# Optimization experiments

Measured on AMD Instinct MI355X. Metric: run time of the kernel, lower is better.

The kernel has to match this reference:

```python
import jax, jax.numpy as jnp
import numpy as np

B, D, S, U, H = 2, 1024, 2048, 1024, 16
LN_EPS = 1e-5

def setup_inputs() -> dict:
    key = jax.random.key(0)
    ks = jax.random.split(key, 5)
    std = 0.02
    return {
        "inputs": jax.random.normal(ks[0], (B, D, S), jnp.float32),
        "Wq": jax.random.normal(ks[1], (D, U), jnp.float32) * std,
        "bq": jnp.zeros((U,), jnp.float32),
        "Wk": jax.random.normal(ks[2], (D, U), jnp.float32) * std,
        "bk": jnp.zeros((U,), jnp.float32),
        "Wv": jax.random.normal(ks[3], (D, U), jnp.float32) * std,
        "bv": jnp.zeros((U,), jnp.float32),
        "Wo": jax.random.normal(ks[4], (U, D), jnp.float32) * std,
        "bo": jnp.zeros((D,), jnp.float32),
        "gamma": jnp.ones((D,), jnp.float32),
        "beta": jnp.zeros((D,), jnp.float32),
        "num_heads": H,
    }

def reference(inputs, Wq, bq, Wk, bk, Wv, bv, Wo, bo, gamma, beta, num_heads):
    # inputs: (B, D, S) -> (B, S, D)
    x = jnp.transpose(inputs, (0, 2, 1))
    b, s, d = x.shape

    def proj(W, bias):
        y = jax.nn.relu(x @ W + bias)               # (b, s, U)
        y = y.reshape(b, s, num_heads, -1)
        return jnp.transpose(y, (0, 2, 1, 3))       # (b, h, s, hd)

    Q = proj(Wq, bq)
    K = proj(Wk, bk)
    V = proj(Wv, bv)
    hd = Q.shape[-1]
    scale = 1.0 / np.sqrt(hd).astype(np.float32)

    # Block-wise flash attention in the source is mathematically plain softmax attention
    # (per-block epsilon 1e-10 is negligible); scale applied to Q, no mask, no dropout.
    scores = jnp.einsum('bhid,bhjd->bhij', Q * scale, K)   # (b, h, s, s)
    P = jax.nn.softmax(scores, axis=-1)
    O = jnp.einsum('bhij,bhjd->bhid', P, V)                # (b, h, s, hd)

    O = jnp.transpose(O, (0, 2, 1, 3)).reshape(b, s, -1)   # (b, s, U)
    out = O @ Wo + bo + x                                  # residual add
    mean = jnp.mean(out, axis=-1, keepdims=True)
    var = jnp.var(out, axis=-1, keepdims=True)
    y = (out - mean) * jax.lax.rsqrt(var + LN_EPS) * gamma + beta
    return jnp.transpose(y, (0, 2, 1))                     # (B, D, S)
```

## Files before the change

kernel.cpp:

```cpp
#include <hip/hip_runtime.h>
#include <hip/hip_bf16.h>

typedef __bf16 bf16x8 __attribute__((ext_vector_type(8)));
typedef __bf16 bf16x4 __attribute__((ext_vector_type(4)));
typedef float  f32x4  __attribute__((ext_vector_type(4)));
typedef float  f32x16 __attribute__((ext_vector_type(16)));

#define MFMA16(a, b, c) __builtin_amdgcn_mfma_f32_16x16x32_bf16((a), (b), (c), 0, 0, 0)
#define MFMA32(a, b, c) __builtin_amdgcn_mfma_f32_32x32x16_bf16((a), (b), (c), 0, 0, 0)

namespace {
constexpr int Bb = 2, Dd = 1024, Ss = 2048, Uu = 1024, Hh = 16;
}

#if __has_builtin(__builtin_amdgcn_exp2f)
#define EXP2(x) __builtin_amdgcn_exp2f(x)
#else
#define EXP2(x) __expf((x) * 0.6931471805599453f)
#endif

__device__ __forceinline__ uint32_t pkbf(float a, float b) {
  union { __bf16 h[2]; uint32_t u; } z;
  z.h[0] = (__bf16)a; z.h[1] = (__bf16)b;
  return z.u;
}
#define PLSWAP(a, b) asm("v_permlane32_swap_b32 %0, %1" : "+v"(a), "+v"(b))

__device__ __forceinline__ void gl16(const void* g, void* l) {
  __builtin_amdgcn_global_load_lds((const __attribute__((address_space(1))) uint32_t*)g,
                                   (__attribute__((address_space(3))) uint32_t*)l, 16, 0, 0);
}

#define VMW(n) asm volatile("s_waitcnt vmcnt(" #n ")" ::: "memory")
#define BARRIER_PIN() do { __builtin_amdgcn_s_barrier(); \
  asm volatile("" ::: "memory"); __builtin_amdgcn_sched_barrier(0); } while (0)
#define LGKM0() asm volatile("s_waitcnt lgkmcnt(0)" ::: "memory")

__global__ __launch_bounds__(256) void k_xpose_x(const float* __restrict__ inp,
                                                 __bf16* __restrict__ xb, float* __restrict__ xt) {
  __shared__ __attribute__((aligned(16))) float xs[64][65];
  const int s0 = blockIdx.x * 64, d0 = blockIdx.y * 64, b = blockIdx.z;
  const int t = threadIdx.x;
  {
    const int i = t >> 2, c = (t & 3) * 16;
    const float* src = inp + ((size_t)(b * Dd + d0 + i)) * Ss + s0 + c;
#pragma unroll
    for (int q = 0; q < 4; ++q) {
      const float4 f = *(const float4*)(src + q * 4);
      xs[i][c + q * 4 + 0] = f.x; xs[i][c + q * 4 + 1] = f.y;
      xs[i][c + q * 4 + 2] = f.z; xs[i][c + q * 4 + 3] = f.w;
    }
  }
  __syncthreads();
  {
    const int sl = t >> 2, dc = (t & 3) * 16;
    float* dstf = xt + ((size_t)(b * Ss + s0 + sl)) * Dd + d0 + dc;
    bf16x8 va, vb;
#pragma unroll
    for (int q = 0; q < 4; ++q) {
      float4 f;
      f.x = xs[dc + q * 4 + 0][sl]; f.y = xs[dc + q * 4 + 1][sl];
      f.z = xs[dc + q * 4 + 2][sl]; f.w = xs[dc + q * 4 + 3][sl];
      *(float4*)(dstf + q * 4) = f;
    }
#pragma unroll
    for (int j = 0; j < 8; ++j) { va[j] = (__bf16)xs[dc + j][sl]; vb[j] = (__bf16)xs[dc + 8 + j][sl]; }
    __bf16* dst = xb + ((size_t)(b * Ss + s0 + sl)) * Dd + d0 + dc;
    *(bf16x8*)dst = va;
    *(bf16x8*)(dst + 8) = vb;
  }
}

__global__ __launch_bounds__(256) void k_xpose_w(const float* __restrict__ w0, const float* __restrict__ w1,
                                                 const float* __restrict__ w2, const float* __restrict__ w3,
                                                 __bf16* __restrict__ o0, __bf16* __restrict__ o1,
                                                 __bf16* __restrict__ o2, __bf16* __restrict__ o3) {
  __shared__ __attribute__((aligned(16))) __bf16 ts[64][72];
  const float* src_m; __bf16* dst_m;
  switch (blockIdx.z) {
    case 0: src_m = w0; dst_m = o0; break;
    case 1: src_m = w1; dst_m = o1; break;
    case 2: src_m = w2; dst_m = o2; break;
    default: src_m = w3; dst_m = o3; break;
  }
  const int n0 = blockIdx.x * 64, k0 = blockIdx.y * 64;
  const int t = threadIdx.x;
  {
    const int i = t >> 2, c = (t & 3) * 16;
    const float* src = src_m + (size_t)(k0 + i) * 1024 + n0 + c;
#pragma unroll
    for (int q = 0; q < 4; ++q) {
      const float4 f = *(const float4*)(src + q * 4);
      ts[i][c + q * 4 + 0] = (__bf16)f.x;
      ts[i][c + q * 4 + 1] = (__bf16)f.y;
      ts[i][c + q * 4 + 2] = (__bf16)f.z;
      ts[i][c + q * 4 + 3] = (__bf16)f.w;
    }
  }
  __syncthreads();
  {
    const int nl = t >> 2, kc = (t & 3) * 16;
    bf16x8 va, vb;
#pragma unroll
    for (int j = 0; j < 8; ++j) { va[j] = ts[kc + j][nl]; vb[j] = ts[kc + 8 + j][nl]; }
    __bf16* dst = dst_m + (size_t)(n0 + nl) * 1024 + k0 + kc;
    *(bf16x8*)dst = va;
    *(bf16x8*)(dst + 8) = vb;
  }
}

__global__ __launch_bounds__(512, 2) void k_gemm_qkv8(const __bf16* __restrict__ A,
    const __bf16* __restrict__ W0, const __bf16* __restrict__ W1, const __bf16* __restrict__ W2,
    const float* __restrict__ b0, const float* __restrict__ b1, const float* __restrict__ b2,
    __bf16* __restrict__ Qb, __bf16* __restrict__ Kb, __bf16* __restrict__ Vt) {
  __shared__ __attribute__((aligned(16))) __bf16 As[4][256][32];
  __shared__ __attribute__((aligned(16))) __bf16 Bs[4][256][32];
  const int t = threadIdx.x;
  const int w = t >> 6, l = t & 63, lg = l >> 4, lr = l & 15;
  const int wm = w >> 2, wn = w & 3;
  const int bid = blockIdx.x;
  const int logical = (bid & 7) * 24 + (bid >> 3);
  const int z = logical >> 6;
  const int rem = logical & 63;
  const int n0 = (rem & 3) * 256, m0 = (rem >> 2) * 256;
  const __bf16* Bt = z == 0 ? W0 : z == 1 ? W1 : W2;
  const float* bias = z == 0 ? b0 : z == 1 ? b1 : b2;

  const int srow = t >> 2, sc8 = t & 3, scol = sc8 * 8;
  const int so = ((sc8 + 4 - ((srow >> 1) & 3)) & 3) * 8;
  const __bf16* gaB = A  + ((size_t)(m0 + srow)) * 1024 + so;
  const __bf16* gbB = Bt + ((size_t)(n0 + srow)) * 1024 + so;
#define STG_A(s, h, kt) gl16(gaB + (size_t)(h) * 128 * 1024 + (kt) * 32, &As[s][(h) * 128 + srow][scol])
#define STG_B(s, h, kt) gl16(gbB + (size_t)(h) * 128 * 1024 + (kt) * 32, &Bs[s][(h) * 128 + srow][scol])

  STG_A(0, 0, 0); STG_A(0, 1, 0); STG_B(0, 0, 0); STG_B(0, 1, 0);
  STG_A(1, 0, 1); STG_A(1, 1, 1); STG_B(1, 0, 1); STG_B(1, 1, 1);
  STG_A(2, 0, 2); STG_A(2, 1, 2); STG_B(2, 0, 2); STG_B(2, 1, 2);
  f32x4 acc[8][4] = {};
  VMW(8);
  BARRIER_PIN();

  const int rdc = ((lg + (lr >> 1)) & 3) * 8;
  const __bf16* Abase = &As[0][0][0] + wm * 4096 + lr * 32 + rdc;
  const __bf16* Bbase = &Bs[0][0][0] + wn * 2048 + lr * 32 + rdc;

  for (int kt = 0; kt < 32; ++kt) {
    const int sC = kt & 3, sS = (kt + 3) & 3;
    const __bf16* Ap = Abase + sC * 8192;
    const __bf16* Bp = Bbase + sC * 8192;
    bf16x8 a0, a1, a2, a3, bb0, bb1, bb2, bb3;
    a0 = *(const bf16x8*)(Ap);         a1 = *(const bf16x8*)(Ap + 512);
    a2 = *(const bf16x8*)(Ap + 1024);  a3 = *(const bf16x8*)(Ap + 1536);
    bb0 = *(const bf16x8*)(Bp);        bb1 = *(const bf16x8*)(Bp + 512);
    bb2 = *(const bf16x8*)(Bp + 1024); bb3 = *(const bf16x8*)(Bp + 1536);
    if (kt < 29) { STG_A(sS, 0, kt + 3); STG_A(sS, 1, kt + 3); }
    BARRIER_PIN();
    LGKM0(); __builtin_amdgcn_sched_barrier(0);
    __builtin_amdgcn_s_setprio(1);
    acc[0][0] = MFMA16(a0, bb0, acc[0][0]); acc[0][1] = MFMA16(a0, bb1, acc[0][1]);
    acc[0][2] = MFMA16(a0, bb2, acc[0][2]); acc[0][3] = MFMA16(a0, bb3, acc[0][3]);
    acc[1][0] = MFMA16(a1, bb0, acc[1][0]); acc[1][1] = MFMA16(a1, bb1, acc[1][1]);
    acc[1][2] = MFMA16(a1, bb2, acc[1][2]); acc[1][3] = MFMA16(a1, bb3, acc[1][3]);
    acc[2][0] = MFMA16(a2, bb0, acc[2][0]); acc[2][1] = MFMA16(a2, bb1, acc[2][1]);
    acc[2][2] = MFMA16(a2, bb2, acc[2][2]); acc[2][3] = MFMA16(a2, bb3, acc[2][3]);
    acc[3][0] = MFMA16(a3, bb0, acc[3][0]); acc[3][1] = MFMA16(a3, bb1, acc[3][1]);
    acc[3][2] = MFMA16(a3, bb2, acc[3][2]); acc[3][3] = MFMA16(a3, bb3, acc[3][3]);
    __builtin_amdgcn_s_setprio(0);
    BARRIER_PIN();
    a0 = *(const bf16x8*)(Ap + 2048);  a1 = *(const bf16x8*)(Ap + 2560);
    a2 = *(const bf16x8*)(Ap + 3072);  a3 = *(const bf16x8*)(Ap + 3584);
    if (kt < 29) { STG_B(sS, 0, kt + 3); STG_B(sS, 1, kt + 3); }
    if (kt < 29) { VMW(8); } else if (kt == 29) { VMW(4); } else if (kt == 30) { VMW(0); }
    BARRIER_PIN();
    LGKM0(); __builtin_amdgcn_sched_barrier(0);
    __builtin_amdgcn_s_setprio(1);
    acc[4][0] = MFMA16(a0, bb0, acc[4][0]); acc[4][1] = MFMA16(a0, bb1, acc[4][1]);
    acc[4][2] = MFMA16(a0, bb2, acc[4][2]); acc[4][3] = MFMA16(a0, bb3, acc[4][3]);
    acc[5][0] = MFMA16(a1, bb0, acc[5][0]); acc[5][1] = MFMA16(a1, bb1, acc[5][1]);
    acc[5][2] = MFMA16(a1, bb2, acc[5][2]); acc[5][3] = MFMA16(a1, bb3, acc[5][3]);
    acc[6][0] = MFMA16(a2, bb0, acc[6][0]); acc[6][1] = MFMA16(a2, bb1, acc[6][1]);
    acc[6][2] = MFMA16(a2, bb2, acc[6][2]); acc[6][3] = MFMA16(a2, bb3, acc[6][3]);
    acc[7][0] = MFMA16(a3, bb0, acc[7][0]); acc[7][1] = MFMA16(a3, bb1, acc[7][1]);
    acc[7][2] = MFMA16(a3, bb2, acc[7][2]); acc[7][3] = MFMA16(a3, bb3, acc[7][3]);
    __builtin_amdgcn_s_setprio(0);
    BARRIER_PIN();
  }
#undef STG_A
#undef STG_B

  const int b = m0 >> 11, sb = m0 & 2047;
  __bf16* Ct = &As[0][0][0];
  float bi[4];
#pragma unroll
  for (int j = 0; j < 4; ++j) bi[j] = bias[n0 + wn * 64 + j * 16 + lr];
  if (z < 2) {
    __bf16* out = z == 0 ? Qb : Kb;
    const float scale = z == 0 ? 0.125f * 1.44269504f : 1.0f;
    const int h0 = n0 >> 6;
    for (int c = 0; c < 4; ++c) {
      __syncthreads();
      if (wm == (c >> 1)) {
        const int q = c & 1;
#pragma unroll
        for (int j = 0; j < 4; ++j) {
          const int nl = wn * 64 + j * 16 + lr;
#pragma unroll
          for (int i2 = 0; i2 < 4; ++i2)
#pragma unroll
            for (int r = 0; r < 4; ++r)
              Ct[(i2 * 16 + lg * 4 + r) * 264 + nl] =
                  (__bf16)(fmaxf(acc[q * 4 + i2][j][r] + bi[j], 0.0f) * scale);
        }
      }
      __syncthreads();
#pragma unroll
      for (int u4 = 0; u4 < 4; ++u4) {
        const int u = u4 * 512 + t;
        const int sl = u >> 5, ru = u & 31;
        const int hh = ru >> 3, sg = ru & 7;
        const bf16x8 v = *(const bf16x8*)&Ct[sl * 264 + hh * 64 + sg * 8];
        *(bf16x8*)(out + ((size_t)(b * Hh + h0 + hh) * Ss + sb + c * 64 + sl) * 64 + sg * 8) = v;
      }
    }
  } else {
    for (int c = 0; c < 4; ++c) {
      __syncthreads();
      if (wn == c) {
#pragma unroll
        for (int j = 0; j < 4; ++j) {
          const int nli = j * 16 + lr;
#pragma unroll
          for (int mi = 0; mi < 8; ++mi)
#pragma unroll
            for (int r2 = 0; r2 < 4; r2 += 2) {
              const int ml = wm * 128 + mi * 16 + lg * 4 + r2;
              const uint32_t pk = pkbf(fmaxf(acc[mi][j][r2] + bi[j], 0.0f),
                                       fmaxf(acc[mi][j][r2 + 1] + bi[j], 0.0f));
              *(uint32_t*)&Ct[nli * 264 + ml] = pk;
            }
        }
      }
      __syncthreads();
#pragma unroll
      for (int u4 = 0; u4 < 4; ++u4) {
        const int u = u4 * 512 + t;
        const int nl = u >> 5, sg = u & 31;
        const bf16x8 v = *(const bf16x8*)&Ct[nl * 264 + sg * 8];
        *(bf16x8*)(Vt + (size_t)(b * 1024 + n0 + c * 64 + nl) * Ss + sb + sg * 8) = v;
      }
    }
  }
}

__device__ __forceinline__ int swz_slot(int row, int slot) { return (slot + (row >> 1)) & 3; }

__device__ __forceinline__ void gemm_core(const __bf16* __restrict__ A, const __bf16* __restrict__ Bt,
                                          __bf16 (*__restrict__ As)[128][32], __bf16 (*__restrict__ Bs)[128][32],
                                          int m0, int n0, int t, f32x4 acc[4][4]) {
  const int w = t >> 6, l = t & 63;
  const int wm = (w >> 1) * 64, wn = (w & 1) * 64;
  const int lg = l >> 4, lr = l & 15;
  const int sr = t >> 2, sc8 = t & 3;
  const int so = ((sc8 + 4 - ((sr >> 1) & 3)) & 3) * 8;
  const __bf16* ga = A + (size_t)(m0 + sr) * 1024 + so;
  const __bf16* gb = Bt + (size_t)(n0 + sr) * 1024 + so;
  const int de = sr * 32 + sc8 * 8;
#define STG(bf, kk) { \
    gl16(ga + (kk) * 32,             &As[bf][0][0] + de); \
    gl16(ga + (kk) * 32 + 64 * 1024, &As[bf][0][0] + de + 64 * 32); \
    gl16(gb + (kk) * 32,             &Bs[bf][0][0] + de); \
    gl16(gb + (kk) * 32 + 64 * 1024, &Bs[bf][0][0] + de + 64 * 32); }
  STG(0, 0) STG(1, 1)
  for (int s = 0; s < 32; ++s) {
    if (s < 31) { VMW(4); } else { VMW(0); }
    BARRIER_PIN();
    if (s + 2 < 32) { const int b2 = (s + 2) % 3; STG(b2, s + 2) }
    const int cb = s % 3;
    bf16x8 af[4], bfr[4];
#pragma unroll
    for (int i = 0; i < 4; ++i) { const int rr = wm + i * 16 + lr; af[i]  = *(const bf16x8*)&As[cb][rr][swz_slot(rr, lg) * 8]; }
#pragma unroll
    for (int i = 0; i < 4; ++i) { const int rr = wn + i * 16 + lr; bfr[i] = *(const bf16x8*)&Bs[cb][rr][swz_slot(rr, lg) * 8]; }
#pragma unroll
    for (int i = 0; i < 4; ++i)
#pragma unroll
      for (int j = 0; j < 4; ++j) acc[i][j] = MFMA16(af[i], bfr[j], acc[i][j]);
  }
#undef STG
}

__global__ __launch_bounds__(256) void k_gemm_o(const __bf16* __restrict__ A, const __bf16* __restrict__ Bt,
                                                const float* __restrict__ bias, const float* __restrict__ xt,
                                                float* __restrict__ Wb, float* __restrict__ partials) {
  __shared__ __attribute__((aligned(16))) char smem[49152];
  auto As = (__bf16 (*)[128][32])smem;
  auto Bs = (__bf16 (*)[128][32])(smem + 24576);
  float* Cs = (float*)smem;
  const int flat = blockIdx.x;
  const int logical = (flat & 7) * 32 + (flat >> 3);
  const int n0 = (logical & 7) * 128, m0 = (logical >> 3) * 128;
  const int t = threadIdx.x, w = t >> 6, l = t & 63;
  const int wm = (w >> 1) * 64, wn = (w & 1) * 64;
  const int lg = l >> 4, lr = l & 15;
  f32x4 acc[4][4] = {};
  gemm_core(A, Bt, As, Bs, m0, n0, t, acc);
  const int sub = t & 31, rid0 = t >> 5;
#pragma unroll
  for (int h2 = 0; h2 < 2; ++h2) {
    __syncthreads();
    if ((w >> 1) == h2) {
#pragma unroll
      for (int j = 0; j < 4; ++j) {
        const int nl = wn + j * 16 + lr;
        const float bi = bias[n0 + nl];
#pragma unroll
        for (int i = 0; i < 4; ++i)
#pragma unroll
          for (int r = 0; r < 4; ++r)
            Cs[(i * 16 + lg * 4 + r) * 132 + nl] = acc[i][j][r] + bi;
      }
    }
    __syncthreads();
#pragma unroll
    for (int p = 0; p < 8; ++p) {
      const int row = p * 8 + rid0;
      const int m = m0 + h2 * 64 + row;
      float4 v = *(const float4*)&Cs[row * 132 + sub * 4];
      const float4 x4 = *(const float4*)&xt[(size_t)m * 1024 + n0 + sub * 4];
      v.x += x4.x; v.y += x4.y; v.z += x4.z; v.w += x4.w;
      *(float4*)&Wb[(size_t)m * 1024 + n0 + sub * 4] = v;
      float s = v.x + v.y + v.z + v.w;
      float q = v.x * v.x + v.y * v.y + v.z * v.z + v.w * v.w;
      s += __shfl_xor(s, 1); s += __shfl_xor(s, 2); s += __shfl_xor(s, 4); s += __shfl_xor(s, 8);
      q += __shfl_xor(q, 1); q += __shfl_xor(q, 2); q += __shfl_xor(q, 4); q += __shfl_xor(q, 8);
      if ((sub & 15) == 0) {
        const int ci = (n0 >> 6) + (sub >> 4);
        partials[((size_t)m * 16 + ci) * 2]     = s;
        partials[((size_t)m * 16 + ci) * 2 + 1] = q;
      }
    }
  }
}

__global__ __launch_bounds__(256, 2) void k_attn6(const __bf16* __restrict__ Qg, const __bf16* __restrict__ Kg,
                                                  const __bf16* __restrict__ Vt, __bf16* __restrict__ Og) {
  __shared__ __attribute__((aligned(16))) char smem[36864];
  auto Ks = (__bf16 (*)[64][72])smem;
  auto Vs = (__bf16 (*)[64][72])(smem + 18432);
  __bf16* Os = (__bf16*)smem;
  const int t = threadIdx.x, l = t & 63, w = t >> 6;
  const int ln = l & 31, hi = l >> 5;
  const int bid = blockIdx.x;
  const int orig = (bid & 7) * 64 + (bid >> 3);
  const int bh = orig >> 4, qt = orig & 15;
  const int q0blk = qt * 128;
  const int q0w = q0blk + w * 32;
  const int b = bh >> 4, h = bh & 15;
  const size_t kbase = (size_t)bh * Ss * 64;
  const int srow = t >> 2, scol = (t & 3) * 16;
  const __bf16* Krow = Kg + kbase + (size_t)srow * 64 + scol;
  const __bf16* Vrow = Vt + (size_t)(bh * 64 + srow) * Ss + scol;

  bf16x8 qf0, qf1, qf2, qf3;
  {
    const __bf16* qp = Qg + kbase + (size_t)(q0w + ln) * 64 + hi * 8;
    qf0 = *(const bf16x8*)(qp);
    qf1 = *(const bf16x8*)(qp + 16);
    qf2 = *(const bf16x8*)(qp + 32);
    qf3 = *(const bf16x8*)(qp + 48);
  }
  f32x16 oA = {}, oB = {};
  float lrow = 0.f;

  auto tile_compute = [&](const __bf16 (&K)[64][72], const __bf16 (&V)[64][72]) {
    f32x16 s0 = {}, s1 = {};
    {
      bf16x8 kf;
#define QK(u, cc, sacc) \
      kf = *(const bf16x8*)&K[(u) * 32 + ln][(cc) * 16 + hi * 8]; \
      sacc = MFMA32(kf, qf##cc, sacc);
      QK(0, 0, s0) QK(0, 1, s0) QK(0, 2, s0) QK(0, 3, s0)
      QK(1, 0, s1) QK(1, 1, s1) QK(1, 2, s1) QK(1, 3, s1)
#undef QK
    }
#pragma unroll
    for (int r = 0; r < 16; ++r) s0[r] = EXP2(s0[r]);
#pragma unroll
    for (int r = 0; r < 16; ++r) s1[r] = EXP2(s1[r]);
    float sm[16];
#pragma unroll
    for (int r = 0; r < 8; ++r) sm[r] = s0[2 * r] + s0[2 * r + 1];
#pragma unroll
    for (int r = 0; r < 8; ++r) sm[8 + r] = s1[2 * r] + s1[2 * r + 1];
#pragma unroll
    for (int st = 8; st > 0; st >>= 1)
#pragma unroll
      for (int r = 0; r < st; ++r) sm[r] += sm[r + st];
    lrow += sm[0];
    uint32_t w0[8], w1[8];
#pragma unroll
    for (int k = 0; k < 8; ++k) w0[k] = pkbf(s0[2 * k], s0[2 * k + 1]);
#pragma unroll
    for (int k = 0; k < 8; ++k) w1[k] = pkbf(s1[2 * k], s1[2 * k + 1]);
    PLSWAP(w0[0], w0[2]); PLSWAP(w0[1], w0[3]);
    PLSWAP(w0[4], w0[6]); PLSWAP(w0[5], w0[7]);
    PLSWAP(w1[0], w1[2]); PLSWAP(w1[1], w1[3]);
    PLSWAP(w1[4], w1[6]); PLSWAP(w1[5], w1[7]);
    union U4 { uint32_t u[4]; bf16x8 v; };
    U4 z;
    bf16x8 pa0, pa1, pa2, pa3;
    z.u[0] = w0[0]; z.u[1] = w0[1]; z.u[2] = w0[2]; z.u[3] = w0[3]; pa0 = z.v;
    z.u[0] = w0[4]; z.u[1] = w0[5]; z.u[2] = w0[6]; z.u[3] = w0[7]; pa1 = z.v;
    z.u[0] = w1[0]; z.u[1] = w1[1]; z.u[2] = w1[2]; z.u[3] = w1[3]; pa2 = z.v;
    z.u[0] = w1[4]; z.u[1] = w1[5]; z.u[2] = w1[6]; z.u[3] = w1[7]; pa3 = z.v;
    {
      bf16x8 vf;
#define PV(half, ti, pa, oacc) \
      vf = *(const bf16x8*)&V[(half) * 32 + ln][(ti) * 16 + hi * 8]; \
      oacc = MFMA32(vf, pa, oacc);
      PV(0, 0, pa0, oA) PV(0, 1, pa1, oA) PV(0, 2, pa2, oA) PV(0, 3, pa3, oA)
      PV(1, 0, pa0, oB) PV(1, 1, pa1, oB) PV(1, 2, pa2, oB) PV(1, 3, pa3, oB)
#undef PV
    }
  };

  bf16x8 kA0 = *(const bf16x8*)(Krow),      kA1 = *(const bf16x8*)(Krow + 8);
  bf16x8 vA0 = *(const bf16x8*)(Vrow),      vA1 = *(const bf16x8*)(Vrow + 8);
  bf16x8 kB0 = *(const bf16x8*)(Krow + 64 * 64), kB1 = *(const bf16x8*)(Krow + 64 * 64 + 8);
  bf16x8 vB0 = *(const bf16x8*)(Vrow + 64), vB1 = *(const bf16x8*)(Vrow + 64 + 8);

  for (int tt = 0; tt < 16; ++tt) {
    *(bf16x8*)&Ks[0][srow][scol]     = kA0;
    *(bf16x8*)&Ks[0][srow][scol + 8] = kA1;
    *(bf16x8*)&Vs[0][srow][scol]     = vA0;
    *(bf16x8*)&Vs[0][srow][scol + 8] = vA1;
    LGKM0();
    BARRIER_PIN();
    if (tt < 15) {
      const size_t ko = (size_t)(2 * tt + 2) * 64;
      kA0 = *(const bf16x8*)(Krow + ko * 64);
      kA1 = *(const bf16x8*)(Krow + ko * 64 + 8);
      vA0 = *(const bf16x8*)(Vrow + ko);
      vA1 = *(const bf16x8*)(Vrow + ko + 8);
    }
    tile_compute(Ks[0], Vs[0]);
    *(bf16x8*)&Ks[1][srow][scol]     = kB0;
    *(bf16x8*)&Ks[1][srow][scol + 8] = kB1;
    *(bf16x8*)&Vs[1][srow][scol]     = vB0;
    *(bf16x8*)&Vs[1][srow][scol + 8] = vB1;
    LGKM0();
    BARRIER_PIN();
    if (tt < 15) {
      const size_t ko = (size_t)(2 * tt + 3) * 64;
      kB0 = *(const bf16x8*)(Krow + ko * 64);
      kB1 = *(const bf16x8*)(Krow + ko * 64 + 8);
      vB0 = *(const bf16x8*)(Vrow + ko);
      vB1 = *(const bf16x8*)(Vrow + ko + 8);
    }
    tile_compute(Ks[1], Vs[1]);
  }
  {
    uint32_t a = __builtin_bit_cast(uint32_t, lrow), bsw = a;
    PLSWAP(a, bsw);
    lrow = __builtin_bit_cast(float, a) + __builtin_bit_cast(float, bsw);
  }
  const float rl = 1.0f / lrow;
  __syncthreads();
  const int ql = w * 32 + ln;
#pragma unroll
  for (int r0 = 0; r0 < 4; ++r0)
#pragma unroll
    for (int j = 0; j < 4; ++j) {
      Os[ql * 68 + hi * 4 + r0 * 8 + j]      = (__bf16)(oA[r0 * 4 + j] * rl);
      Os[ql * 68 + 32 + hi * 4 + r0 * 8 + j] = (__bf16)(oB[r0 * 4 + j] * rl);
    }
  __syncthreads();
  const int sub = t & 7, rid0 = t >> 3;
#pragma unroll
  for (int p = 0; p < 4; ++p) {
    const int rid = p * 32 + rid0;
    const bf16x8 v = *(const bf16x8*)&Os[rid * 68 + sub * 8];
    *(bf16x8*)(Og + ((size_t)(b * Ss + q0blk + rid)) * Uu + h * 64 + sub * 8) = v;
  }
}

__global__ __launch_bounds__(256) void k_ln_stats(const float* __restrict__ partials, float* __restrict__ stats) {
  const int row = blockIdx.x * 256 + threadIdx.x;
  float s = 0.f, q = 0.f;
#pragma unroll
  for (int c = 0; c < 16; ++c) {
    s += partials[((size_t)row * 16 + c) * 2];
    q += partials[((size_t)row * 16 + c) * 2 + 1];
  }
  const float mean = s * (1.0f / 1024.0f);
  const float var = q * (1.0f / 1024.0f) - mean * mean;
  stats[row * 2] = mean;
  stats[row * 2 + 1] = rsqrtf(var + 1e-5f);
}

__global__ __launch_bounds__(256) void k_ln_write(const float* __restrict__ Wb, const float* __restrict__ stats,
                                                  const float* __restrict__ gamma, const float* __restrict__ beta,
                                                  float* __restrict__ out) {
  __shared__ __attribute__((aligned(16))) float ws0[64][65];
  __shared__ float sm[64][2];
  const int d0 = blockIdx.x * 64, s0 = blockIdx.y * 64, b = blockIdx.z;
  const int t = threadIdx.x;
  {
    const int sl = t >> 2, dc = (t & 3) * 16;
    const float* src = Wb + ((size_t)(b * Ss + s0 + sl)) * Dd + d0 + dc;
#pragma unroll
    for (int q = 0; q < 4; ++q) {
      const float4 f = *(const float4*)(src + q * 4);
      ws0[dc + q * 4 + 0][sl] = f.x; ws0[dc + q * 4 + 1][sl] = f.y;
      ws0[dc + q * 4 + 2][sl] = f.z; ws0[dc + q * 4 + 3][sl] = f.w;
    }
  }
  if (t < 128) sm[t >> 1][t & 1] = stats[(size_t)(b * Ss + s0 + (t >> 1)) * 2 + (t & 1)];
  __syncthreads();
  const int dl = t >> 2, sc = (t & 3) * 16;
  const float g = gamma[d0 + dl], be = beta[d0 + dl];
  float* dst = out + ((size_t)(b * Dd + d0 + dl)) * Ss + s0 + sc;
#pragma unroll
  for (int q = 0; q < 4; ++q) {
    float4 o;
    o.x = (ws0[dl][sc + q * 4 + 0] - sm[sc + q * 4 + 0][0]) * sm[sc + q * 4 + 0][1] * g + be;
    o.y = (ws0[dl][sc + q * 4 + 1] - sm[sc + q * 4 + 1][0]) * sm[sc + q * 4 + 1][1] * g + be;
    o.z = (ws0[dl][sc + q * 4 + 2] - sm[sc + q * 4 + 2][0]) * sm[sc + q * 4 + 2][1] * g + be;
    o.w = (ws0[dl][sc + q * 4 + 3] - sm[sc + q * 4 + 3][0]) * sm[sc + q * 4 + 3][1] * g + be;
    *(float4*)(dst + q * 4) = o;
  }
}

extern "C" void kernel_launch(void* const* d_in, const int* in_sizes, int n_in,
                              void* d_out, int out_size, void* d_ws, size_t ws_size,
                              hipStream_t stream) {
  const float* inp   = (const float*)d_in[0];
  const float* Wq    = (const float*)d_in[1];
  const float* bq    = (const float*)d_in[2];
  const float* Wk    = (const float*)d_in[3];
  const float* bk    = (const float*)d_in[4];
  const float* Wv    = (const float*)d_in[5];
  const float* bv    = (const float*)d_in[6];
  const float* Wo    = (const float*)d_in[7];
  const float* bo    = (const float*)d_in[8];
  const float* gamma = (const float*)d_in[9];
  const float* beta  = (const float*)d_in[10];

  char* ws = (char*)d_ws;
  const size_t MB = 1ull << 20;
  __bf16* xb  = (__bf16*)(ws);
  __bf16* Wqt = (__bf16*)(ws + 8 * MB);
  __bf16* Wkt = (__bf16*)(ws + 10 * MB);
  __bf16* Wvt = (__bf16*)(ws + 12 * MB);
  __bf16* Wot = (__bf16*)(ws + 14 * MB);
  __bf16* Qb  = (__bf16*)(ws + 16 * MB);
  __bf16* Kb  = (__bf16*)(ws + 24 * MB);
  __bf16* Vtb = (__bf16*)(ws + 32 * MB);
  __bf16* Ob  = (__bf16*)(ws + 40 * MB);
  float*  xt  = (float*)(ws + 48 * MB);
  float*  Wb  = (float*)(ws + 16 * MB);
  float*  partials = (float*)(ws + 8 * MB);
  float*  stats    = (float*)(ws + 8 * MB + 512 * 1024);

  k_xpose_x<<<dim3(32, 16, 2), 256, 0, stream>>>(inp, xb, xt);
  k_xpose_w<<<dim3(16, 16, 4), 256, 0, stream>>>(Wq, Wk, Wv, Wo, Wqt, Wkt, Wvt, Wot);
  k_gemm_qkv8<<<dim3(192), 512, 0, stream>>>(xb, Wqt, Wkt, Wvt, bq, bk, bv, Qb, Kb, Vtb);
  k_attn6<<<dim3(512), 256, 0, stream>>>(Qb, Kb, Vtb, Ob);
  k_gemm_o<<<dim3(256), 256, 0, stream>>>(Ob, Wot, bo, xt, Wb, partials);
  k_ln_stats<<<dim3(16), 256, 0, stream>>>(partials, stats);
  k_ln_write<<<dim3(16, 32, 2), 256, 0, stream>>>(Wb, stats, gamma, beta, (float*)d_out);
}
```

Before: 141.2 us.

## Split attention over two KV halves with combine pass; keep residual and pre-LN in bf16

The attention kernel now splits each head's 2048 keys into two halves, so twice as many blocks run, and it raises the launch-bounds occupancy hint. Each half writes unnormalized outputs and row sums, and a new combine kernel adds the two halves and normalizes them. The fp32 transposed copy of x is dropped: the residual reads the bf16 x, and the pre-LayerNorm buffer is stored in bf16, which roughly halves that intermediate traffic. The costs are an extra kernel and extra global traffic for the partial outputs. The combine is only exact if both halves share the same softmax reference. Keeping the residual and pre-LN activations in bf16 also loses precision.

```diff
diff --git a/kernel.cpp b/kernel.cpp
--- a/kernel.cpp
+++ b/kernel.cpp
@@ -37,8 +37,8 @@
 #define LGKM0() asm volatile("s_waitcnt lgkmcnt(0)" ::: "memory")
 
 __global__ __launch_bounds__(256) void k_xpose_x(const float* __restrict__ inp,
-                                                 __bf16* __restrict__ xb, float* __restrict__ xt) {
-  __shared__ __attribute__((aligned(16))) float xs[64][65];
+                                                 __bf16* __restrict__ xb) {
+  __shared__ __attribute__((aligned(16))) __bf16 ts[64][72];
   const int s0 = blockIdx.x * 64, d0 = blockIdx.y * 64, b = blockIdx.z;
   const int t = threadIdx.x;
   {
@@ -47,24 +47,18 @@
 #pragma unroll
     for (int q = 0; q < 4; ++q) {
       const float4 f = *(const float4*)(src + q * 4);
-      xs[i][c + q * 4 + 0] = f.x; xs[i][c + q * 4 + 1] = f.y;
-      xs[i][c + q * 4 + 2] = f.z; xs[i][c + q * 4 + 3] = f.w;
+      ts[i][c + q * 4 + 0] = (__bf16)f.x;
+      ts[i][c + q * 4 + 1] = (__bf16)f.y;
+      ts[i][c + q * 4 + 2] = (__bf16)f.z;
+      ts[i][c + q * 4 + 3] = (__bf16)f.w;
     }
   }
   __syncthreads();
   {
     const int sl = t >> 2, dc = (t & 3) * 16;
-    float* dstf = xt + ((size_t)(b * Ss + s0 + sl)) * Dd + d0 + dc;
     bf16x8 va, vb;
 #pragma unroll
-    for (int q = 0; q < 4; ++q) {
-      float4 f;
-      f.x = xs[dc + q * 4 + 0][sl]; f.y = xs[dc + q * 4 + 1][sl];
-      f.z = xs[dc + q * 4 + 2][sl]; f.w = xs[dc + q * 4 + 3][sl];
-      *(float4*)(dstf + q * 4) = f;
-    }
-#pragma unroll
-    for (int j = 0; j < 8; ++j) { va[j] = (__bf16)xs[dc + j][sl]; vb[j] = (__bf16)xs[dc + 8 + j][sl]; }
+    for (int j = 0; j < 8; ++j) { va[j] = ts[dc + j][sl]; vb[j] = ts[dc + 8 + j][sl]; }
     __bf16* dst = xb + ((size_t)(b * Ss + s0 + sl)) * Dd + d0 + dc;
     *(bf16x8*)dst = va;
     *(bf16x8*)(dst + 8) = vb;
@@ -290,8 +284,8 @@
 }
 
 __global__ __launch_bounds__(256) void k_gemm_o(const __bf16* __restrict__ A, const __bf16* __restrict__ Bt,
-                                                const float* __restrict__ bias, const float* __restrict__ xt,
-                                                float* __restrict__ Wb, float* __restrict__ partials) {
+                                                const float* __restrict__ bias, const __bf16* __restrict__ xb,
+                                                __bf16* __restrict__ Wb, float* __restrict__ partials) {
   __shared__ __attribute__((aligned(16))) char smem[49152];
   auto As = (__bf16 (*)[128][32])smem;
   auto Bs = (__bf16 (*)[128][32])(smem + 24576);
@@ -326,9 +320,11 @@
       const int row = p * 8 + rid0;
       const int m = m0 + h2 * 64 + row;
       float4 v = *(const float4*)&Cs[row * 132 + sub * 4];
-      const float4 x4 = *(const float4*)&xt[(size_t)m * 1024 + n0 + sub * 4];
-      v.x += x4.x; v.y += x4.y; v.z += x4.z; v.w += x4.w;
-      *(float4*)&Wb[(size_t)m * 1024 + n0 + sub * 4] = v;
+      const bf16x4 x4 = *(const bf16x4*)&xb[(size_t)m * 1024 + n0 + sub * 4];
+      v.x += (float)x4[0]; v.y += (float)x4[1]; v.z += (float)x4[2]; v.w += (float)x4[3];
+      bf16x4 pv;
+      pv[0] = (__bf16)v.x; pv[1] = (__bf16)v.y; pv[2] = (__bf16)v.z; pv[3] = (__bf16)v.w;
+      *(bf16x4*)&Wb[(size_t)m * 1024 + n0 + sub * 4] = pv;
       float s = v.x + v.y + v.z + v.w;
       float q = v.x * v.x + v.y * v.y + v.z * v.z + v.w * v.w;
       s += __shfl_xor(s, 1); s += __shfl_xor(s, 2); s += __shfl_xor(s, 4); s += __shfl_xor(s, 8);
@@ -342,8 +338,10 @@
   }
 }
 
-__global__ __launch_bounds__(256, 2) void k_attn6(const __bf16* __restrict__ Qg, const __bf16* __restrict__ Kg,
-                                                  const __bf16* __restrict__ Vt, __bf16* __restrict__ Og) {
+__global__ __launch_bounds__(256, 4) void k_attn9(const __bf16* __restrict__ Qg, const __bf16* __restrict__ Kg,
+                                                  const __bf16* __restrict__ Vt,
+                                                  __bf16* __restrict__ Op0, __bf16* __restrict__ Op1,
+                                                  float* __restrict__ Lp) {
   __shared__ __attribute__((aligned(16))) char smem[36864];
   auto Ks = (__bf16 (*)[64][72])smem;
   auto Vs = (__bf16 (*)[64][72])(smem + 18432);
@@ -351,15 +349,17 @@
   const int t = threadIdx.x, l = t & 63, w = t >> 6;
   const int ln = l & 31, hi = l >> 5;
   const int bid = blockIdx.x;
-  const int orig = (bid & 7) * 64 + (bid >> 3);
-  const int bh = orig >> 4, qt = orig & 15;
+  const int orig = (bid & 7) * 128 + (bid >> 3);
+  const int bh = orig >> 5;
+  const int rest = orig & 31;
+  const int qt = rest >> 1, kvh = rest & 1;
   const int q0blk = qt * 128;
   const int q0w = q0blk + w * 32;
   const int b = bh >> 4, h = bh & 15;
   const size_t kbase = (size_t)bh * Ss * 64;
   const int srow = t >> 2, scol = (t & 3) * 16;
-  const __bf16* Krow = Kg + kbase + (size_t)srow * 64 + scol;
-  const __bf16* Vrow = Vt + (size_t)(bh * 64 + srow) * Ss + scol;
+  const __bf16* Krow = Kg + kbase + (size_t)(kvh * 1024 + srow) * 64 + scol;
+  const __bf16* Vrow = Vt + (size_t)(bh * 64 + srow) * Ss + kvh * 1024 + scol;
 
   bf16x8 qf0, qf1, qf2, qf3;
   {
@@ -424,19 +424,19 @@
     }
   };
 
-  bf16x8 kA0 = *(const bf16x8*)(Krow),      kA1 = *(const bf16x8*)(Krow + 8);
-  bf16x8 vA0 = *(const bf16x8*)(Vrow),      vA1 = *(const bf16x8*)(Vrow + 8);
+  bf16x8 kA0 = *(const bf16x8*)(Krow),           kA1 = *(const bf16x8*)(Krow + 8);
+  bf16x8 vA0 = *(const bf16x8*)(Vrow),           vA1 = *(const bf16x8*)(Vrow + 8);
   bf16x8 kB0 = *(const bf16x8*)(Krow + 64 * 64), kB1 = *(const bf16x8*)(Krow + 64 * 64 + 8);
-  bf16x8 vB0 = *(const bf16x8*)(Vrow + 64), vB1 = *(const bf16x8*)(Vrow + 64 + 8);
-
-  for (int tt = 0; tt < 16; ++tt) {
+  bf16x8 vB0 = *(const bf16x8*)(Vrow + 64),      vB1 = *(const bf16x8*)(Vrow + 64 + 8);
+
+  for (int tt = 0; tt < 8; ++tt) {
     *(bf16x8*)&Ks[0][srow][scol]     = kA0;
     *(bf16x8*)&Ks[0][srow][scol + 8] = kA1;
     *(bf16x8*)&Vs[0][srow][scol]     = vA0;
     *(bf16x8*)&Vs[0][srow][scol + 8] = vA1;
     LGKM0();
     BARRIER_PIN();
-    if (tt < 15) {
+    if (tt < 7) {
       const size_t ko = (size_t)(2 * tt + 2) * 64;
       kA0 = *(const bf16x8*)(Krow + ko * 64);
       kA1 = *(const bf16x8*)(Krow + ko * 64 + 8);
@@ -450,7 +450,7 @@
     *(bf16x8*)&Vs[1][srow][scol + 8] = vB1;
     LGKM0();
     BARRIER_PIN();
-    if (tt < 15) {
+    if (tt < 7) {
       const size_t ko = (size_t)(2 * tt + 3) * 64;
       kB0 = *(const bf16x8*)(Krow + ko * 64);
       kB1 = *(const bf16x8*)(Krow + ko * 64 + 8);
@@ -464,24 +464,43 @@
     PLSWAP(a, bsw);
     lrow = __builtin_bit_cast(float, a) + __builtin_bit_cast(float, bsw);
   }
-  const float rl = 1.0f / lrow;
+  if (hi == 0)
+    Lp[(size_t)kvh * 65536 + (size_t)bh * 2048 + q0w + ln] = lrow;
   __syncthreads();
   const int ql = w * 32 + ln;
 #pragma unroll
   for (int r0 = 0; r0 < 4; ++r0)
 #pragma unroll
     for (int j = 0; j < 4; ++j) {
-      Os[ql * 68 + hi * 4 + r0 * 8 + j]      = (__bf16)(oA[r0 * 4 + j] * rl);
-      Os[ql * 68 + 32 + hi * 4 + r0 * 8 + j] = (__bf16)(oB[r0 * 4 + j] * rl);
+      Os[ql * 68 + hi * 4 + r0 * 8 + j]      = (__bf16)(oA[r0 * 4 + j]);
+      Os[ql * 68 + 32 + hi * 4 + r0 * 8 + j] = (__bf16)(oB[r0 * 4 + j]);
     }
   __syncthreads();
+  __bf16* Op = kvh ? Op1 : Op0;
   const int sub = t & 7, rid0 = t >> 3;
 #pragma unroll
   for (int p = 0; p < 4; ++p) {
     const int rid = p * 32 + rid0;
     const bf16x8 v = *(const bf16x8*)&Os[rid * 68 + sub * 8];
-    *(bf16x8*)(Og + ((size_t)(b * Ss + q0blk + rid)) * Uu + h * 64 + sub * 8) = v;
-  }
+    *(bf16x8*)(Op + ((size_t)(b * Ss + q0blk + rid)) * Uu + h * 64 + sub * 8) = v;
+  }
+}
+
+__global__ __launch_bounds__(256) void k_combine(const __bf16* __restrict__ Op0, const __bf16* __restrict__ Op1,
+                                                 const float* __restrict__ Lp, __bf16* __restrict__ Og) {
+  const size_t idx = (size_t)blockIdx.x * 256 + threadIdx.x;
+  const size_t e0 = idx * 8;
+  const int row = (int)(e0 >> 10);
+  const int d = (int)(e0 & 1023);
+  const int b = row >> 11, s = row & 2047, h = d >> 6;
+  const size_t lidx = ((size_t)(b * 16 + h)) * 2048 + s;
+  const float rl = 1.0f / (Lp[lidx] + Lp[65536 + lidx]);
+  const bf16x8 a = *(const bf16x8*)(Op0 + e0);
+  const bf16x8 c = *(const bf16x8*)(Op1 + e0);
+  bf16x8 o;
+#pragma unroll
+  for (int j = 0; j < 8; ++j) o[j] = (__bf16)(((float)a[j] + (float)c[j]) * rl);
+  *(bf16x8*)(Og + e0) = o;
 }
 
 __global__ __launch_bounds__(256) void k_ln_stats(const float* __restrict__ partials, float* __restrict__ stats) {
@@ -498,7 +517,7 @@
   stats[row * 2 + 1] = rsqrtf(var + 1e-5f);
 }
 
-__global__ __launch_bounds__(256) void k_ln_write(const float* __restrict__ Wb, const float* __restrict__ stats,
+__global__ __launch_bounds__(256) void k_ln_write(const __bf16* __restrict__ Wb, const float* __restrict__ stats,
                                                   const float* __restrict__ gamma, const float* __restrict__ beta,
                                                   float* __restrict__ out) {
   __shared__ __attribute__((aligned(16))) float ws0[64][65];
@@ -507,13 +526,11 @@
   const int t = threadIdx.x;
   {
     const int sl = t >> 2, dc = (t & 3) * 16;
-    const float* src = Wb + ((size_t)(b * Ss + s0 + sl)) * Dd + d0 + dc;
-#pragma unroll
-    for (int q = 0; q < 4; ++q) {
-      const float4 f = *(const float4*)(src + q * 4);
-      ws0[dc + q * 4 + 0][sl] = f.x; ws0[dc + q * 4 + 1][sl] = f.y;
-      ws0[dc + q * 4 + 2][sl] = f.z; ws0[dc + q * 4 + 3][sl] = f.w;
-    }
+    const __bf16* src = Wb + ((size_t)(b * Ss + s0 + sl)) * Dd + d0 + dc;
+    const bf16x8 f0 = *(const bf16x8*)src;
+    const bf16x8 f1 = *(const bf16x8*)(src + 8);
+#pragma unroll
+    for (int j = 0; j < 8; ++j) { ws0[dc + j][sl] = (float)f0[j]; ws0[dc + 8 + j][sl] = (float)f1[j]; }
   }
   if (t < 128) sm[t >> 1][t & 1] = stats[(size_t)(b * Ss + s0 + (t >> 1)) * 2 + (t & 1)];
   __syncthreads();
@@ -556,17 +573,20 @@
   __bf16* Qb  = (__bf16*)(ws + 16 * MB);
   __bf16* Kb  = (__bf16*)(ws + 24 * MB);
   __bf16* Vtb = (__bf16*)(ws + 32 * MB);
-  __bf16* Ob  = (__bf16*)(ws + 40 * MB);
-  float*  xt  = (float*)(ws + 48 * MB);
-  float*  Wb  = (float*)(ws + 16 * MB);
+  __bf16* Op0 = (__bf16*)(ws + 40 * MB);
+  __bf16* Op1 = (__bf16*)(ws + 48 * MB);
+  __bf16* Onr = (__bf16*)(ws + 56 * MB);
+  float*  Lp  = (float*)(ws + 9 * MB);
+  __bf16* Wb  = (__bf16*)(ws + 16 * MB);
   float*  partials = (float*)(ws + 8 * MB);
   float*  stats    = (float*)(ws + 8 * MB + 512 * 1024);
 
-  k_xpose_x<<<dim3(32, 16, 2), 256, 0, stream>>>(inp, xb, xt);
+  k_xpose_x<<<dim3(32, 16, 2), 256, 0, stream>>>(inp, xb);
   k_xpose_w<<<dim3(16, 16, 4), 256, 0, stream>>>(Wq, Wk, Wv, Wo, Wqt, Wkt, Wvt, Wot);
   k_gemm_qkv8<<<dim3(192), 512, 0, stream>>>(xb, Wqt, Wkt, Wvt, bq, bk, bv, Qb, Kb, Vtb);
-  k_attn6<<<dim3(512), 256, 0, stream>>>(Qb, Kb, Vtb, Ob);
-  k_gemm_o<<<dim3(256), 256, 0, stream>>>(Ob, Wot, bo, xt, Wb, partials);
+  k_attn9<<<dim3(1024), 256, 0, stream>>>(Qb, Kb, Vtb, Op0, Op1, Lp);
+  k_combine<<<dim3(2048), 256, 0, stream>>>(Op0, Op1, Lp, Onr);
+  k_gemm_o<<<dim3(256), 256, 0, stream>>>(Onr, Wot, bo, xb, Wb, partials);
   k_ln_stats<<<dim3(16), 256, 0, stream>>>(partials, stats);
   k_ln_write<<<dim3(16, 32, 2), 256, 0, stream>>>(Wb, stats, gamma, beta, (float*)d_out);
 }
```

Result: slower. 157.7 us (+11.7%).

## Store residual and pre-LN intermediate in bf16, add MFMA priority hints in attention

Applied to the files above, without the earlier changes.

Drops the fp32 transposed copy of x and reuses the bf16 copy for the residual add. The pre-LayerNorm buffer is now written and read as bf16 instead of fp32, which roughly halves the traffic for those intermediate tensors across several kernels. It also wraps the attention MFMA blocks in s_setprio raises to favour matrix issue. The cost is lower precision in the residual and in the normalized values, which adds error to the output.

```diff
diff --git a/kernel.cpp b/kernel.cpp
--- a/kernel.cpp
+++ b/kernel.cpp
@@ -37,8 +37,8 @@
 #define LGKM0() asm volatile("s_waitcnt lgkmcnt(0)" ::: "memory")
 
 __global__ __launch_bounds__(256) void k_xpose_x(const float* __restrict__ inp,
-                                                 __bf16* __restrict__ xb, float* __restrict__ xt) {
-  __shared__ __attribute__((aligned(16))) float xs[64][65];
+                                                 __bf16* __restrict__ xb) {
+  __shared__ __attribute__((aligned(16))) __bf16 ts[64][72];
   const int s0 = blockIdx.x * 64, d0 = blockIdx.y * 64, b = blockIdx.z;
   const int t = threadIdx.x;
   {
@@ -47,24 +47,18 @@
 #pragma unroll
     for (int q = 0; q < 4; ++q) {
       const float4 f = *(const float4*)(src + q * 4);
-      xs[i][c + q * 4 + 0] = f.x; xs[i][c + q * 4 + 1] = f.y;
-      xs[i][c + q * 4 + 2] = f.z; xs[i][c + q * 4 + 3] = f.w;
+      ts[i][c + q * 4 + 0] = (__bf16)f.x;
+      ts[i][c + q * 4 + 1] = (__bf16)f.y;
+      ts[i][c + q * 4 + 2] = (__bf16)f.z;
+      ts[i][c + q * 4 + 3] = (__bf16)f.w;
     }
   }
   __syncthreads();
   {
     const int sl = t >> 2, dc = (t & 3) * 16;
-    float* dstf = xt + ((size_t)(b * Ss + s0 + sl)) * Dd + d0 + dc;
     bf16x8 va, vb;
 #pragma unroll
-    for (int q = 0; q < 4; ++q) {
-      float4 f;
-      f.x = xs[dc + q * 4 + 0][sl]; f.y = xs[dc + q * 4 + 1][sl];
-      f.z = xs[dc + q * 4 + 2][sl]; f.w = xs[dc + q * 4 + 3][sl];
-      *(float4*)(dstf + q * 4) = f;
-    }
-#pragma unroll
-    for (int j = 0; j < 8; ++j) { va[j] = (__bf16)xs[dc + j][sl]; vb[j] = (__bf16)xs[dc + 8 + j][sl]; }
+    for (int j = 0; j < 8; ++j) { va[j] = ts[dc + j][sl]; vb[j] = ts[dc + 8 + j][sl]; }
     __bf16* dst = xb + ((size_t)(b * Ss + s0 + sl)) * Dd + d0 + dc;
     *(bf16x8*)dst = va;
     *(bf16x8*)(dst + 8) = vb;
@@ -290,8 +284,8 @@
 }
 
 __global__ __launch_bounds__(256) void k_gemm_o(const __bf16* __restrict__ A, const __bf16* __restrict__ Bt,
-                                                const float* __restrict__ bias, const float* __restrict__ xt,
-                                                float* __restrict__ Wb, float* __restrict__ partials) {
+                                                const float* __restrict__ bias, const __bf16* __restrict__ xb,
+                                                __bf16* __restrict__ Wb, float* __restrict__ partials) {
   __shared__ __attribute__((aligned(16))) char smem[49152];
   auto As = (__bf16 (*)[128][32])smem;
   auto Bs = (__bf16 (*)[128][32])(smem + 24576);
@@ -326,9 +320,11 @@
       const int row = p * 8 + rid0;
       const int m = m0 + h2 * 64 + row;
       float4 v = *(const float4*)&Cs[row * 132 + sub * 4];
-      const float4 x4 = *(const float4*)&xt[(size_t)m * 1024 + n0 + sub * 4];
-      v.x += x4.x; v.y += x4.y; v.z += x4.z; v.w += x4.w;
-      *(float4*)&Wb[(size_t)m * 1024 + n0 + sub * 4] = v;
+      const bf16x4 x4 = *(const bf16x4*)&xb[(size_t)m * 1024 + n0 + sub * 4];
+      v.x += (float)x4[0]; v.y += (float)x4[1]; v.z += (float)x4[2]; v.w += (float)x4[3];
+      bf16x4 pv;
+      pv[0] = (__bf16)v.x; pv[1] = (__bf16)v.y; pv[2] = (__bf16)v.z; pv[3] = (__bf16)v.w;
+      *(bf16x4*)&Wb[(size_t)m * 1024 + n0 + sub * 4] = pv;
       float s = v.x + v.y + v.z + v.w;
       float q = v.x * v.x + v.y * v.y + v.z * v.z + v.w * v.w;
       s += __shfl_xor(s, 1); s += __shfl_xor(s, 2); s += __shfl_xor(s, 4); s += __shfl_xor(s, 8);
@@ -374,6 +370,7 @@
 
   auto tile_compute = [&](const __bf16 (&K)[64][72], const __bf16 (&V)[64][72]) {
     f32x16 s0 = {}, s1 = {};
+    __builtin_amdgcn_s_setprio(1);
     {
       bf16x8 kf;
 #define QK(u, cc, sacc) \
@@ -383,6 +380,7 @@
       QK(1, 0, s1) QK(1, 1, s1) QK(1, 2, s1) QK(1, 3, s1)
 #undef QK
     }
+    __builtin_amdgcn_s_setprio(0);
 #pragma unroll
     for (int r = 0; r < 16; ++r) s0[r] = EXP2(s0[r]);
 #pragma unroll
@@ -413,6 +411,7 @@
     z.u[0] = w0[4]; z.u[1] = w0[5]; z.u[2] = w0[6]; z.u[3] = w0[7]; pa1 = z.v;
     z.u[0] = w1[0]; z.u[1] = w1[1]; z.u[2] = w1[2]; z.u[3] = w1[3]; pa2 = z.v;
     z.u[0] = w1[4]; z.u[1] = w1[5]; z.u[2] = w1[6]; z.u[3] = w1[7]; pa3 = z.v;
+    __builtin_amdgcn_s_setprio(1);
     {
       bf16x8 vf;
 #define PV(half, ti, pa, oacc) \
@@ -422,6 +421,7 @@
       PV(1, 0, pa0, oB) PV(1, 1, pa1, oB) PV(1, 2, pa2, oB) PV(1, 3, pa3, oB)
 #undef PV
     }
+    __builtin_amdgcn_s_setprio(0);
   };
 
   bf16x8 kA0 = *(const bf16x8*)(Krow),      kA1 = *(const bf16x8*)(Krow + 8);
@@ -498,7 +498,7 @@
   stats[row * 2 + 1] = rsqrtf(var + 1e-5f);
 }
 
-__global__ __launch_bounds__(256) void k_ln_write(const float* __restrict__ Wb, const float* __restrict__ stats,
+__global__ __launch_bounds__(256) void k_ln_write(const __bf16* __restrict__ Wb, const float* __restrict__ stats,
                                                   const float* __restrict__ gamma, const float* __restrict__ beta,
                                                   float* __restrict__ out) {
   __shared__ __attribute__((aligned(16))) float ws0[64][65];
@@ -507,13 +507,11 @@
   const int t = threadIdx.x;
   {
     const int sl = t >> 2, dc = (t & 3) * 16;
-    const float* src = Wb + ((size_t)(b * Ss + s0 + sl)) * Dd + d0 + dc;
-#pragma unroll
-    for (int q = 0; q < 4; ++q) {
-      const float4 f = *(const float4*)(src + q * 4);
-      ws0[dc + q * 4 + 0][sl] = f.x; ws0[dc + q * 4 + 1][sl] = f.y;
-      ws0[dc + q * 4 + 2][sl] = f.z; ws0[dc + q * 4 + 3][sl] = f.w;
-    }
+    const __bf16* src = Wb + ((size_t)(b * Ss + s0 + sl)) * Dd + d0 + dc;
+    const bf16x8 f0 = *(const bf16x8*)src;
+    const bf16x8 f1 = *(const bf16x8*)(src + 8);
+#pragma unroll
+    for (int j = 0; j < 8; ++j) { ws0[dc + j][sl] = (float)f0[j]; ws0[dc + 8 + j][sl] = (float)f1[j]; }
   }
   if (t < 128) sm[t >> 1][t & 1] = stats[(size_t)(b * Ss + s0 + (t >> 1)) * 2 + (t & 1)];
   __syncthreads();
@@ -557,16 +555,15 @@
   __bf16* Kb  = (__bf16*)(ws + 24 * MB);
   __bf16* Vtb = (__bf16*)(ws + 32 * MB);
   __bf16* Ob  = (__bf16*)(ws + 40 * MB);
-  float*  xt  = (float*)(ws + 48 * MB);
-  float*  Wb  = (float*)(ws + 16 * MB);
+  __bf16* Wb  = (__bf16*)(ws + 16 * MB);
   float*  partials = (float*)(ws + 8 * MB);
   float*  stats    = (float*)(ws + 8 * MB + 512 * 1024);
 
-  k_xpose_x<<<dim3(32, 16, 2), 256, 0, stream>>>(inp, xb, xt);
+  k_xpose_x<<<dim3(32, 16, 2), 256, 0, stream>>>(inp, xb);
   k_xpose_w<<<dim3(16, 16, 4), 256, 0, stream>>>(Wq, Wk, Wv, Wo, Wqt, Wkt, Wvt, Wot);
   k_gemm_qkv8<<<dim3(192), 512, 0, stream>>>(xb, Wqt, Wkt, Wvt, bq, bk, bv, Qb, Kb, Vtb);
   k_attn6<<<dim3(512), 256, 0, stream>>>(Qb, Kb, Vtb, Ob);
-  k_gemm_o<<<dim3(256), 256, 0, stream>>>(Ob, Wot, bo, xt, Wb, partials);
+  k_gemm_o<<<dim3(256), 256, 0, stream>>>(Ob, Wot, bo, xb, Wb, partials);
   k_ln_stats<<<dim3(16), 256, 0, stream>>>(partials, stats);
   k_ln_write<<<dim3(16, 32, 2), 256, 0, stream>>>(Wb, stats, gamma, beta, (float*)d_out);
 }
```

Measured after the change: 134.0 us, median of 2. 5.1% less time.
